# Performance work log

Hardware: AMD Instinct MI355X
Metric: run time of the kernel (lower is better)

## Reference

```python
import jax, jax.numpy as jnp
import numpy as np

V = 20000          # vocab size ('ALL')
E = 512            # embedding_dim
H = 1024           # rnn_hidden_size
LD = 256           # latent_dim
NL = 2             # num_rnn_layers_dec (hidden_factor = 2, unidirectional)
B = 32
S = 256
PAD = 0
CUT0 = 30          # cutoffs = [30, 100, 1000], div_value = 4.0
TAIL_SPECS = [(30, 100, 256), (100, 1000, 64), (1000, V, 16)]  # (low, high, proj_dim)


def setup_inputs() -> dict:
    key = jax.random.key(0)
    ks = jax.random.split(key, 24)
    w = lambda k, shp: (0.02 * jax.random.normal(k, shp)).astype(jnp.float32)

    z = jax.random.normal(ks[0], (B, LD), dtype=jnp.float32)
    emb = w(ks[1], (V, E))
    l2h_w = w(ks[2], (NL * H, LD))
    l2h_b = jnp.zeros((NL * H,), jnp.float32)
    # RNN layer 0 (input E) and layer 1 (input H)
    rnn0_wih = w(ks[3], (H, E)); rnn0_whh = w(ks[4], (H, H))
    rnn0_bih = jnp.zeros((H,), jnp.float32); rnn0_bhh = jnp.zeros((H,), jnp.float32)
    rnn1_wih = w(ks[5], (H, H)); rnn1_whh = w(ks[6], (H, H))
    rnn1_bih = jnp.zeros((H,), jnp.float32); rnn1_bhh = jnp.zeros((H,), jnp.float32)
    # adaptive softmax: head = 30 shortlist + 3 cluster logits
    head_w = w(ks[7], (CUT0 + 3, H))
    tail_p0 = w(ks[8], (256, H));  tail_w0 = w(ks[9], (70, 256))
    tail_p1 = w(ks[10], (64, H));  tail_w1 = w(ks[11], (900, 64))
    tail_p2 = w(ks[12], (16, H));  tail_w2 = w(ks[13], (V - 1000, 16))

    length = jax.random.randint(ks[14], (B,), 32, S + 1)
    pos = jnp.arange(S)[None, :]
    mask = pos < length[:, None]
    inp_seq = jax.random.randint(ks[15], (B, S), 4, V)
    inp_seq = jnp.where(mask, inp_seq, PAD)
    target_seq = jax.random.randint(ks[16], (B, S), 4, V)
    target_seq = jnp.where(mask, target_seq, PAD)

    return dict(z=z, emb=emb, l2h_w=l2h_w, l2h_b=l2h_b,
                rnn0_wih=rnn0_wih, rnn0_whh=rnn0_whh, rnn0_bih=rnn0_bih, rnn0_bhh=rnn0_bhh,
                rnn1_wih=rnn1_wih, rnn1_whh=rnn1_whh, rnn1_bih=rnn1_bih, rnn1_bhh=rnn1_bhh,
                head_w=head_w, tail_p0=tail_p0, tail_w0=tail_w0, tail_p1=tail_p1,
                tail_w1=tail_w1, tail_p2=tail_p2, tail_w2=tail_w2,
                inp_seq=inp_seq, target_seq=target_seq, length=length)


def _rnn_layer(x, h0, wih, whh, bih, bhh):
    # x: [B,S,D], h0: [B,H] -> [B,S,H]  (tanh vanilla RNN)
    def step(h, xt):
        h = jnp.tanh(xt @ wih.T + bih + h @ whh.T + bhh)
        return h, h
    _, ys = jax.lax.scan(step, h0, jnp.swapaxes(x, 0, 1))
    return jnp.swapaxes(ys, 0, 1)


def _adaptive_log_prob(x, head_w, tails):
    # x: [N,H] -> full log-probs [N,V] (AdaptiveLogSoftmaxWithLoss.log_prob)
    head_lp = jax.nn.log_softmax(x @ head_w.T, axis=-1)  # [N, 33]
    parts = [head_lp[:, :CUT0]]
    for i, (p, w) in enumerate(tails):
        clp = jax.nn.log_softmax((x @ p.T) @ w.T, axis=-1)
        parts.append(clp + head_lp[:, CUT0 + i][:, None])
    return jnp.concatenate(parts, axis=1)


def reference(z, emb, l2h_w, l2h_b,
              rnn0_wih, rnn0_whh, rnn0_bih, rnn0_bhh,
              rnn1_wih, rnn1_whh, rnn1_bih, rnn1_bhh,
              head_w, tail_p0, tail_w0, tail_p1, tail_w1, tail_p2, tail_w2,
              inp_seq, target_seq, length):
    # sort inputs by descending length (hidden is NOT sorted, as in the original)
    sorted_idx = jnp.argsort(-length)
    x = emb[inp_seq[sorted_idx]]                         # [B,S,E]
    hid = z @ l2h_w.T + l2h_b                            # [B, 2H]
    hidden = hid.reshape(NL, B, H)                       # torch .view(hidden_factor, B, H)
    h1 = _rnn_layer(x, hidden[0], rnn0_wih, rnn0_whh, rnn0_bih, rnn0_bhh)
    h2 = _rnn_layer(h1, hidden[1], rnn1_wih, rnn1_whh, rnn1_bih, rnn1_bhh)
    rev = jnp.argsort(sorted_idx)
    out = h2[rev].reshape(-1, H)                         # [N,H]
    tgt = target_seq.reshape(-1)                         # [N]
    lp = _adaptive_log_prob(out, head_w,
                            [(tail_p0, tail_w0), (tail_p1, tail_w1), (tail_p2, tail_w2)])
    nll = -jnp.take_along_axis(lp, tgt[:, None], axis=1)[:, 0]
    nll = jnp.where(tgt == PAD, 0.0, nll)
    return jnp.sum(nll)
```

## Files before the change

### kernel.cpp

```cpp
#include <hip/hip_runtime.h>
#include <hip/hip_bf16.h>
#include <math.h>

#define BB 32
#define SS 256
#define EE 512
#define HH 1024
#define LDM 256
#define NROW (BB*SS)
#define NWG 64

typedef __attribute__((ext_vector_type(8))) short bf16x8;
typedef __attribute__((ext_vector_type(4))) float f32x4;
typedef unsigned long long u64;

static __device__ inline unsigned short f2bf(float f){
  unsigned u = __float_as_uint(f);
  unsigned r = (u + 0x7fffu + ((u >> 16) & 1u)) >> 16;
  return (unsigned short)r;
}
static __device__ inline unsigned short f2bf_fast(float f){
  return (unsigned short)((__float_as_uint(f) + 0x8000u) >> 16);
}
static __device__ inline bf16x8 cvt8(float4 x, float4 y){
  union { ushort s[8]; bf16x8 v; } t;
  t.s[0]=f2bf_fast(x.x); t.s[1]=f2bf_fast(x.y); t.s[2]=f2bf_fast(x.z); t.s[3]=f2bf_fast(x.w);
  t.s[4]=f2bf_fast(y.x); t.s[5]=f2bf_fast(y.y); t.s[6]=f2bf_fast(y.z); t.s[7]=f2bf_fast(y.w);
  return t.v;
}
static __device__ inline unsigned packbf(float a, float b){
  return (unsigned)f2bf(a) | ((unsigned)f2bf(b) << 16);
}

static __device__ inline float ftanh(float x){
  float e = __expf(2.f*x);
  return 1.f - 2.f/(e + 1.f);
}

#define GLD(dst, p) asm volatile("global_load_dwordx4 %0, %1, off sc0 sc1" \
                                 : "=v"(dst) : "v"(p) : "memory")

static __device__ inline bf16x8 asbf(f32x4 x){
  union { f32x4 f; bf16x8 b; } u; u.f = x; return u.b;
}

__global__ void k_sort(const int* __restrict__ length, int* __restrict__ sorted_idx){
  int b = threadIdx.x;
  if (b >= BB) return;
  int lb = length[b];
  int r = 0;
  for (int o = 0; o < BB; ++o){
    int lo = length[o];
    if (lo > lb || (lo == lb && o < b)) ++r;
  }
  sorted_idx[r] = b;
}

__global__ void k_maps(const int* __restrict__ sorted_idx,
                       const int* __restrict__ inp_seq, const int* __restrict__ tgt_seq,
                       int* __restrict__ tokmap, int* __restrict__ tgtmap){
  int bs = blockIdx.x; int t = threadIdx.x;
  int b = sorted_idx[bs];
  tokmap[bs*SS + t] = inp_seq[b*SS + t];
  tgtmap[bs*SS + t] = tgt_seq[b*SS + t];
}

__global__ __launch_bounds__(256) void k_hid(const float* __restrict__ z,
        const float* __restrict__ w, const float* __restrict__ bias,
        ushort* __restrict__ hb0){
  int id = blockIdx.x*256 + threadIdx.x;
  int b = id >> 11, c = id & 2047;
  const float4* zr = (const float4*)(z + b*LDM);
  const float4* wr = (const float4*)(w + (size_t)c*LDM);
  float a0=0,a1=0,a2=0,a3=0;
  #pragma unroll 4
  for (int k=0;k<LDM/4;k++){ float4 zz=zr[k], ww=wr[k];
    a0+=zz.x*ww.x; a1+=zz.y*ww.y; a2+=zz.z*ww.z; a3+=zz.w*ww.w; }
  float val = a0+a1+a2+a3 + bias[c];
  int layer = id >> 15, bp = (id >> 10) & 31, j = id & 1023;
  hb0[(layer<<15) + ((j>>3)<<8) + (bp<<3) + (j&7)] = f2bf(val);
}

__global__ __launch_bounds__(256) void k_wcat(
    const float* __restrict__ head_w, const float* __restrict__ p0,
    const float* __restrict__ p1, const float* __restrict__ p2,
    float* __restrict__ wcat){
  int row = blockIdx.x; int t = threadIdx.x;
  float4* dst = (float4*)(wcat + (size_t)row*HH);
  const float* src;
  if      (row < 33)  src = head_w + (size_t)row*HH;
  else if (row < 289) src = p0 + (size_t)(row-33)*HH;
  else if (row < 353) src = p1 + (size_t)(row-289)*HH;
  else if (row < 369) src = p2 + (size_t)(row-353)*HH;
  else { dst[t] = make_float4(0.f,0.f,0.f,0.f); return; }
  dst[t] = ((const float4*)src)[t];
}

__global__ __launch_bounds__(256) void k_bin(
    const int* __restrict__ tgtmap, int* __restrict__ cnt,
    int* __restrict__ l0, int* __restrict__ l1, int* __restrict__ l2)
{
  int row = blockIdx.x*256 + threadIdx.x;
  int tgt = tgtmap[row];
  int ci = (tgt == 0) ? -1 : (tgt >= 1000) ? 2 : (tgt >= 100) ? 1 : (tgt >= 30) ? 0 : -1;
  int lane = threadIdx.x & 63;
  #pragma unroll
  for (int c = 0; c < 3; ++c){
    unsigned long long mask = __ballot(ci == c);
    int nc = __popcll(mask);
    int base = 0;
    if (lane == 0 && nc) base = atomicAdd(&cnt[c], nc);
    base = __shfl(base, 0);
    if (ci == c){
      int pos = __popcll(mask & ((1ull << lane) - 1ull));
      int* lst = (c == 0) ? l0 : (c == 1) ? l1 : l2;
      lst[base + pos] = row;
    }
  }
}

__global__ __launch_bounds__(256) void k_gemm_bf16(
    const float* __restrict__ A, int lda, const int* __restrict__ rowmap, int abf16,
    const float* __restrict__ Bm,
    const float* __restrict__ bias0, const float* __restrict__ bias1,
    float* __restrict__ C, int M, int N, int K)
{
  __shared__ ushort As[128*72];
  __shared__ ushort Bs[128*72];
  const int nt = blockIdx.x * 128, mt = blockIdx.y * 128;
  const int tid = threadIdx.x;
  const int wv = tid >> 6, ln = tid & 63;
  const int wm = wv & 1, wn = wv >> 1;
  const int lc = ln & 15, quad = ln >> 4;
  f32x4 acc[4][4] = {{{0.f,0.f,0.f,0.f}}};

  for (int s = 0; s < K; s += 64){
    __syncthreads();
    #pragma unroll
    for (int cc = 0; cc < 4; ++cc){
      int ch = tid*4 + cc;
      int r = ch >> 3, c = ch & 7;
      int ar = mt + r;
      if (abf16){
        const ushort* ap = (const ushort*)A + (size_t)ar*lda + s + c*8;
        *(bf16x8*)&As[r*72 + c*8] = *(const bf16x8*)ap;
      } else {
        const float* ap = A + (size_t)(rowmap ? rowmap[ar] : ar)*lda + s + c*8;
        float4 x = *(const float4*)ap, y = *(const float4*)(ap+4);
        *(bf16x8*)&As[r*72 + c*8] = cvt8(x, y);
      }
      int br = nt + r; if (br >= N) br = N - 1;
      const float* bp = Bm + (size_t)br*K + s + c*8;
      float4 bx = *(const float4*)bp, by = *(const float4*)(bp+4);
      *(bf16x8*)&Bs[r*72 + c*8] = cvt8(bx, by);
    }
    __syncthreads();
    #pragma unroll
    for (int kq = 0; kq < 2; ++kq){
      int cq = kq*4 + quad;
      bf16x8 af[4], bfv[4];
      #pragma unroll
      for (int i=0;i<4;i++) af[i]  = *(const bf16x8*)&As[(wm*64 + i*16 + lc)*72 + cq*8];
      #pragma unroll
      for (int j=0;j<4;j++) bfv[j] = *(const bf16x8*)&Bs[(wn*64 + j*16 + lc)*72 + cq*8];
      #pragma unroll
      for (int i=0;i<4;i++)
        #pragma unroll
        for (int j=0;j<4;j++)
          acc[i][j] = __builtin_amdgcn_mfma_f32_16x16x32_bf16(af[i], bfv[j], acc[i][j], 0, 0, 0);
    }
  }
  #pragma unroll
  for (int j=0;j<4;j++){
    int col = nt + wn*64 + j*16 + lc;
    if (col < N){
      float badd = (bias0 ? bias0[col] : 0.f) + (bias1 ? bias1[col] : 0.f);
      #pragma unroll
      for (int i=0;i<4;i++){
        int row = mt + wm*64 + i*16 + quad*4;
        #pragma unroll
        for (int r=0;r<4;r++)
          C[(size_t)(row+r)*N + col] = acc[i][j][r] + badd;
      }
    }
  }
}

__global__ __launch_bounds__(256, 1) void k_rnn_fused(
    const float* __restrict__ pre0, ushort* __restrict__ h2out,
    const float* __restrict__ w0hh, const float* __restrict__ w1ih,
    const float* __restrict__ w1hh,
    const float* __restrict__ b1ih, const float* __restrict__ b1hh,
    const ushort* __restrict__ hb0, ushort* __restrict__ hx, int* flags)
{
  __shared__ ushort w0F[16384], wiF[16384], whF[16384];
  __shared__ float red[4352];
  const int wg  = blockIdx.x;
  const int tid = threadIdx.x;
  const int j0  = wg * 16;
  int* ctr = flags + (wg & 7) * 32;

  for (int c = tid; c < 4096; c += 256){
    int rr = c >> 8, cc = (c & 255) * 4;
    int dst = ((cc >> 3)*16 + rr)*8 + (cc & 7);
    size_t srow = (size_t)(j0 + rr)*HH + cc;
    float4 w4; uint2 p;
    w4 = *(const float4*)&w0hh[srow];
    p.x = packbf(w4.x, w4.y); p.y = packbf(w4.z, w4.w);
    *(uint2*)&w0F[dst] = p;
    w4 = *(const float4*)&w1ih[srow];
    p.x = packbf(w4.x, w4.y); p.y = packbf(w4.z, w4.w);
    *(uint2*)&wiF[dst] = p;
    w4 = *(const float4*)&w1hh[srow];
    p.x = packbf(w4.x, w4.y); p.y = packbf(w4.z, w4.w);
    *(uint2*)&whF[dst] = p;
  }
  const int lane = tid & 63, wv = tid >> 6;
  const int col = lane & 15, quad = lane >> 4;
  const int ob = tid >> 3, oj = (tid << 1) & 15;

  float2 pre = *(const float2*)&pre0[((size_t)ob*SS + 0)*HH + j0 + oj];
  float2 pre2;
  pre2.x = b1ih[j0+oj]   + b1hh[j0+oj];
  pre2.y = b1ih[j0+oj+1] + b1hh[j0+oj+1];
  __syncthreads();

  for (int r = 0; r < SS; ++r){
    const u64* s1 = (const u64*)(r == 0 ? hb0 : hx + ((r-1)&1)*32768);
    const u64* s2 = (r == 0) ? (const u64*)hb0
                  : (const u64*)(r == 1 ? hb0 + 32768 : hx + (2 + (r&1))*32768);
    f32x4 a0r[8], a1r[8], c0r[8], c1r[8];
    #pragma unroll
    for (int ks = 0; ks < 8; ++ks){
      int kb = wv*32 + ks*4 + quad;
      const u64* p = s1 + (kb << 6) + (col << 1);
      GLD(a0r[ks], p);
      GLD(a1r[ks], p + 32);
    }
    if (r > 0){
      #pragma unroll
      for (int ks = 0; ks < 8; ++ks){
        int kb = wv*32 + ks*4 + quad;
        const u64* p = s2 + (kb << 6) + (col << 1);
        GLD(c0r[ks], p);
        GLD(c1r[ks], p + 32);
      }
    }
    asm volatile("s_waitcnt vmcnt(0)" ::: "memory");
    __builtin_amdgcn_sched_barrier(0);

    f32x4 accA0 = {0.f,0.f,0.f,0.f}, accA1 = {0.f,0.f,0.f,0.f};
    f32x4 accB0 = {0.f,0.f,0.f,0.f}, accB1 = {0.f,0.f,0.f,0.f};
    #pragma unroll
    for (int ks = 0; ks < 8; ++ks){
      int kb = wv*32 + ks*4 + quad;
      bf16x8 b0 = *(const bf16x8*)&w0F[(kb*16 + col)*8];
      accA0 = __builtin_amdgcn_mfma_f32_16x16x32_bf16(asbf(a0r[ks]), b0, accA0, 0, 0, 0);
      accA1 = __builtin_amdgcn_mfma_f32_16x16x32_bf16(asbf(a1r[ks]), b0, accA1, 0, 0, 0);
      bf16x8 bi = *(const bf16x8*)&wiF[(kb*16 + col)*8];
      accB0 = __builtin_amdgcn_mfma_f32_16x16x32_bf16(asbf(a0r[ks]), bi, accB0, 0, 0, 0);
      accB1 = __builtin_amdgcn_mfma_f32_16x16x32_bf16(asbf(a1r[ks]), bi, accB1, 0, 0, 0);
    }
    if (r > 0){
      #pragma unroll
      for (int ks = 0; ks < 8; ++ks){
        int kb = wv*32 + ks*4 + quad;
        bf16x8 bh = *(const bf16x8*)&whF[(kb*16 + col)*8];
        accB0 = __builtin_amdgcn_mfma_f32_16x16x32_bf16(asbf(c0r[ks]), bh, accB0, 0, 0, 0);
        accB1 = __builtin_amdgcn_mfma_f32_16x16x32_bf16(asbf(c1r[ks]), bh, accB1, 0, 0, 0);
      }
    }
    #pragma unroll
    for (int q = 0; q < 4; ++q){
      red[wv*544 + (quad*4 + q)*17 + col]             = accA0[q];
      red[wv*544 + (16 + quad*4 + q)*17 + col]        = accA1[q];
      red[2176 + wv*544 + (quad*4 + q)*17 + col]      = accB0[q];
      red[2176 + wv*544 + (16 + quad*4 + q)*17 + col] = accB1[q];
    }
    __syncthreads();

    int ro = ob*17 + oj;
    float s0 = red[ro]   + red[544 + ro]   + red[1088 + ro]   + red[1632 + ro];
    float s1v= red[ro+1] + red[544 + ro+1] + red[1088 + ro+1] + red[1632 + ro+1];
    float v0 = ftanh(pre.x + s0);
    float v1 = ftanh(pre.y + s1v);
    int k = j0 + oj;
    unsigned off = ((unsigned)(k >> 3) << 7) + ((unsigned)ob << 2) + ((unsigned)(k & 7) >> 1);
    __hip_atomic_store((unsigned*)(hx + (r&1)*32768) + off, packbf(v0, v1),
                       __ATOMIC_RELAXED, __HIP_MEMORY_SCOPE_AGENT);
    unsigned pk2 = 0;
    if (r > 0){
      float s2v = red[2176+ro]   + red[2720+ro]   + red[3264+ro]   + red[3808+ro];
      float s3v = red[2176+ro+1] + red[2720+ro+1] + red[3264+ro+1] + red[3808+ro+1];
      pk2 = packbf(ftanh(pre2.x + s2v), ftanh(pre2.y + s3v));
      __hip_atomic_store((unsigned*)(hx + (2 + ((r-1)&1))*32768) + off, pk2,
                         __ATOMIC_RELAXED, __HIP_MEMORY_SCOPE_AGENT);
    }
    asm volatile("s_waitcnt vmcnt(0)" ::: "memory");
    __syncthreads();
    if (tid == 0)
      __hip_atomic_fetch_add(ctr, 1, __ATOMIC_RELAXED, __HIP_MEMORY_SCOPE_AGENT);

    if (r > 0)
      *((unsigned*)h2out + (((size_t)ob*SS + (r-1))*HH + j0 + oj) / 2) = pk2;
    int tn = (r + 1 < SS) ? r + 1 : SS - 1;
    pre = *(const float2*)&pre0[((size_t)ob*SS + tn)*HH + j0 + oj];

    if (tid < 8){
      int tv = 8 * (r + 1);
      while (__hip_atomic_load(flags + tid*32, __ATOMIC_RELAXED,
                               __HIP_MEMORY_SCOPE_AGENT) < tv) {}
    }
    __syncthreads();
  }

  {
    const u64* s1 = (const u64*)(hx + 32768);
    const u64* s2 = (const u64*)(hx + 2*32768);
    f32x4 a0r[8], a1r[8], c0r[8], c1r[8];
    #pragma unroll
    for (int ks = 0; ks < 8; ++ks){
      int kb = wv*32 + ks*4 + quad;
      const u64* p1 = s1 + (kb << 6) + (col << 1);
      GLD(a0r[ks], p1); GLD(a1r[ks], p1 + 32);
      const u64* p2 = s2 + (kb << 6) + (col << 1);
      GLD(c0r[ks], p2); GLD(c1r[ks], p2 + 32);
    }
    asm volatile("s_waitcnt vmcnt(0)" ::: "memory");
    __builtin_amdgcn_sched_barrier(0);
    f32x4 accB0 = {0.f,0.f,0.f,0.f}, accB1 = {0.f,0.f,0.f,0.f};
    #pragma unroll
    for (int ks = 0; ks < 8; ++ks){
      int kb = wv*32 + ks*4 + quad;
      bf16x8 bi = *(const bf16x8*)&wiF[(kb*16 + col)*8];
      accB0 = __builtin_amdgcn_mfma_f32_16x16x32_bf16(asbf(a0r[ks]), bi, accB0, 0, 0, 0);
      accB1 = __builtin_amdgcn_mfma_f32_16x16x32_bf16(asbf(a1r[ks]), bi, accB1, 0, 0, 0);
      bf16x8 bh = *(const bf16x8*)&whF[(kb*16 + col)*8];
      accB0 = __builtin_amdgcn_mfma_f32_16x16x32_bf16(asbf(c0r[ks]), bh, accB0, 0, 0, 0);
      accB1 = __builtin_amdgcn_mfma_f32_16x16x32_bf16(asbf(c1r[ks]), bh, accB1, 0, 0, 0);
    }
    #pragma unroll
    for (int q = 0; q < 4; ++q){
      red[wv*544 + (quad*4 + q)*17 + col]      = accB0[q];
      red[wv*544 + (16 + quad*4 + q)*17 + col] = accB1[q];
    }
    __syncthreads();
    int ro = ob*17 + oj;
    float s2v = red[ro]   + red[544 + ro]   + red[1088 + ro]   + red[1632 + ro];
    float s3v = red[ro+1] + red[544 + ro+1] + red[1088 + ro+1] + red[1632 + ro+1];
    *((unsigned*)h2out + (((size_t)ob*SS + (SS-1))*HH + j0 + oj) / 2) =
        packbf(ftanh(pre2.x + s2v), ftanh(pre2.y + s3v));
  }
}

__global__ __launch_bounds__(256) void k_cluster(
    const float* __restrict__ combo, int off, int ld, int Kp,
    const float* __restrict__ W, int Nc,
    const int* __restrict__ rowlist, const int* __restrict__ cntp, int ci,
    float* __restrict__ stats)
{
  __shared__ float ps[4][4][256];
  int lane = threadIdx.x & 63;
  int wvl  = threadIdx.x >> 6;
  int n0 = (blockIdx.x*4 + wvl) * 4;
  int count = cntp[ci];
  int rows[4];
  #pragma unroll
  for (int r=0;r<4;r++){
    rows[r] = (n0 + r < count) ? rowlist[n0 + r] : -1;
    if (rows[r] >= 0)
      for (int k=lane;k<Kp;k+=64)
        ps[wvl][r][k] = combo[(size_t)rows[r]*ld + off + k];
  }
  __syncthreads();
  if (rows[0] < 0) return;

  float mx[4], sm[4];
  #pragma unroll
  for (int r=0;r<4;r++){ mx[r]=-1e30f; sm[r]=0.f; }
  for (int n=lane; n<Nc; n+=64){
    const float* wr = W + (size_t)n*Kp;
    float l[4]={0.f,0.f,0.f,0.f};
    for (int k=0;k<Kp;k+=4){
      float4 w4 = *(const float4*)(wr+k);
      #pragma unroll
      for (int r=0;r<4;r++){
        l[r] += w4.x*ps[wvl][r][k] + w4.y*ps[wvl][r][k+1]
              + w4.z*ps[wvl][r][k+2] + w4.w*ps[wvl][r][k+3];
      }
    }
    #pragma unroll
    for (int r=0;r<4;r++){
      float nm = fmaxf(mx[r], l[r]);
      sm[r] = sm[r]*__expf(mx[r]-nm) + __expf(l[r]-nm);
      mx[r] = nm;
    }
  }
  #pragma unroll
  for (int r=0;r<4;r++){
    for (int off2=32; off2; off2>>=1){
      float om = __shfl_down(mx[r], off2);
      float os = __shfl_down(sm[r], off2);
      float nm = fmaxf(mx[r], om);
      sm[r] = sm[r]*__expf(mx[r]-nm) + os*__expf(om-nm);
      mx[r] = nm;
    }
    if (lane==0 && rows[r] >= 0){
      stats[(size_t)rows[r]*6 + ci*2 + 0] = mx[r];
      stats[(size_t)rows[r]*6 + ci*2 + 1] = sm[r];
    }
  }
}

__global__ __launch_bounds__(256) void k_tlogit(
    const int* __restrict__ tgtmap, const float* __restrict__ combo,
    const float* __restrict__ w0, const float* __restrict__ w1, const float* __restrict__ w2,
    float* __restrict__ tlogit)
{
  int lane = threadIdx.x & 63;
  int row = (blockIdx.x * 256 + threadIdx.x) >> 6;
  int tgt = tgtmap[row];
  float acc = 0.f;
  const float* pr = nullptr; const float* wr = nullptr; int Kp = 0;
  const float* crow = combo + (size_t)row*384;
  if      (tgt >= 1000){ pr = crow + 353; wr = w2 + (size_t)(tgt-1000)*16;  Kp=16;  }
  else if (tgt >= 100) { pr = crow + 289; wr = w1 + (size_t)(tgt-100)*64;   Kp=64;  }
  else if (tgt >= 30)  { pr = crow + 33;  wr = w0 + (size_t)(tgt-30)*256;   Kp=256; }
  for (int k=lane; k<Kp; k+=64) acc += pr[k]*wr[k];
  for (int off=32; off; off>>=1) acc += __shfl_down(acc, off);
  if (lane==0) tlogit[row] = acc;
}

__global__ __launch_bounds__(256) void k_final(
    const float* __restrict__ combo, const float* __restrict__ stats,
    const float* __restrict__ tlogit, const int* __restrict__ tgtmap,
    float* __restrict__ out)
{
  int row = blockIdx.x*256 + threadIdx.x;
  int tgt = tgtmap[row];
  float nll = 0.f;
  if (tgt != 0){
    const float* hrow = combo + (size_t)row*384;
    float m = hrow[0];
    #pragma unroll
    for (int i=1;i<33;i++) m = fmaxf(m, hrow[i]);
    float s = 0.f;
    #pragma unroll
    for (int i=0;i<33;i++) s += __expf(hrow[i]-m);
    float lse = __logf(s) + m;
    int ci = (tgt>=1000) ? 2 : (tgt>=100) ? 1 : (tgt>=30) ? 0 : -1;
    if (ci < 0){
      nll = lse - hrow[tgt];
    } else {
      float cm = stats[(size_t)row*6 + ci*2 + 0];
      float cs = stats[(size_t)row*6 + ci*2 + 1];
      nll = lse - hrow[30+ci] + (__logf(cs) + cm - tlogit[row]);
    }
  }
  float v = nll;
  for (int off=32; off; off>>=1) v += __shfl_down(v, off);
  __shared__ float wsum[4];
  int lane = threadIdx.x & 63, wv = threadIdx.x >> 6;
  if (lane==0) wsum[wv] = v;
  __syncthreads();
  if (threadIdx.x==0) atomicAdd(out, wsum[0]+wsum[1]+wsum[2]+wsum[3]);
}

extern "C" void kernel_launch(void* const* d_in, const int* in_sizes, int n_in,
                              void* d_out, int out_size, void* d_ws, size_t ws_size,
                              hipStream_t stream)
{
  const float* z      = (const float*)d_in[0];
  const float* emb    = (const float*)d_in[1];
  const float* l2h_w  = (const float*)d_in[2];
  const float* l2h_b  = (const float*)d_in[3];
  const float* w0ih   = (const float*)d_in[4];
  const float* w0hh   = (const float*)d_in[5];
  const float* b0ih   = (const float*)d_in[6];
  const float* b0hh   = (const float*)d_in[7];
  const float* w1ih   = (const float*)d_in[8];
  const float* w1hh   = (const float*)d_in[9];
  const float* b1ih   = (const float*)d_in[10];
  const float* b1hh   = (const float*)d_in[11];
  const float* head_w = (const float*)d_in[12];
  const float* p0     = (const float*)d_in[13];
  const float* tw0    = (const float*)d_in[14];
  const float* p1     = (const float*)d_in[15];
  const float* tw1    = (const float*)d_in[16];
  const float* p2     = (const float*)d_in[17];
  const float* tw2    = (const float*)d_in[18];
  const int* inp_seq  = (const int*)d_in[19];
  const int* tgt_seq  = (const int*)d_in[20];
  const int* length   = (const int*)d_in[21];

  float* ws   = (float*)d_ws;
  ushort* hb0 = (ushort*)ws;
  ushort* hx  = hb0 + 65536;
  float* bufA = ws + 98304;
  ushort* hbB = (ushort*)(bufA + (size_t)NROW*HH);
  int*   ibuf = (int*)(hbB + (size_t)NROW*HH);
  int* sorted_idx = ibuf;
  int* tokmap = ibuf + 32;
  int* tgtmap = tokmap + NROW;
  int* flags  = tgtmap + NROW;
  int* bincnt = flags + 512;
  int* blist0 = bincnt + 32;
  int* blist1 = blist0 + NROW;
  int* blist2 = blist1 + NROW;
  float* combo = bufA;
  float* stats = bufA + (size_t)NROW*384;
  float* tlog  = stats + (size_t)NROW*6;
  float* wcat  = tlog + NROW;

  float* outF = (float*)d_out;
  hipMemsetAsync(outF, 0, sizeof(float), stream);
  hipMemsetAsync(flags, 0, 544*sizeof(int), stream);

  k_sort<<<1, 32, 0, stream>>>(length, sorted_idx);
  k_maps<<<32, 256, 0, stream>>>(sorted_idx, inp_seq, tgt_seq, tokmap, tgtmap);
  k_hid<<<256, 256, 0, stream>>>(z, l2h_w, l2h_b, hb0);
  k_bin<<<32, 256, 0, stream>>>(tgtmap, bincnt, blist0, blist1, blist2);

  k_gemm_bf16<<<dim3(HH/128, NROW/128), 256, 0, stream>>>(emb, EE, tokmap, 0, w0ih,
                                                          b0ih, b0hh, bufA, NROW, HH, EE);
  k_rnn_fused<<<NWG, 256, 0, stream>>>(bufA, hbB, w0hh, w1ih, w1hh, b1ih, b1hh,
                                       hb0, hx, flags);

  k_wcat<<<384, 256, 0, stream>>>(head_w, p0, p1, p2, wcat);
  k_gemm_bf16<<<dim3(3, NROW/128), 256, 0, stream>>>((const float*)hbB, HH, nullptr, 1,
                                                     wcat, nullptr, nullptr,
                                                     combo, NROW, 384, HH);

  k_cluster<<<NROW/16, 256, 0, stream>>>(combo, 33,  384, 256, tw0, 70,
                                         blist0, bincnt, 0, stats);
  k_cluster<<<NROW/16, 256, 0, stream>>>(combo, 289, 384, 64,  tw1, 900,
                                         blist1, bincnt, 1, stats);
  k_cluster<<<NROW/16, 256, 0, stream>>>(combo, 353, 384, 16,  tw2, 19000,
                                         blist2, bincnt, 2, stats);
  k_tlogit<<<NROW/4, 256, 0, stream>>>(tgtmap, combo, tw0, tw1, tw2, tlog);
  k_final<<<NROW/256, 256, 0, stream>>>(combo, stats, tlog, tgtmap, outF);
}
```

Measured before the change: 1.529 ms.

## Split fused two-layer RNN into separate layer-1 and layer-2 workgroup roles

The persistent RNN kernel used 64 workgroups that each computed both layers in a skewed wavefront. It now launches 128 workgroups, 64 for layer 1 and 64 for layer 2, which run as a pipeline linked by per-role flag counters and a triple-buffered h1 ring. This halves the per-step MFMA and load work on each workgroup and shortens each step's critical path. In exchange it needs twice as many CUs to be co-resident, adds cross-role spin waits, and enlarges the workspace to hold the extra buffers.

```diff
diff --git a/kernel.cpp b/kernel.cpp
--- a/kernel.cpp
+++ b/kernel.cpp
@@ -8,7 +8,6 @@
 #define HH 1024
 #define LDM 256
 #define NROW (BB*SS)
-#define NWG 64
 
 typedef __attribute__((ext_vector_type(8))) short bf16x8;
 typedef __attribute__((ext_vector_type(4))) float f32x4;
@@ -186,7 +185,7 @@
   }
 }
 
-__global__ __launch_bounds__(256, 1) void k_rnn_fused(
+__global__ __launch_bounds__(256, 1) void k_rnn_split(
     const float* __restrict__ pre0, ushort* __restrict__ h2out,
     const float* __restrict__ w0hh, const float* __restrict__ w1ih,
     const float* __restrict__ w1hh,
@@ -194,162 +193,160 @@
     const ushort* __restrict__ hb0, ushort* __restrict__ hx, int* flags)
 {
   __shared__ ushort w0F[16384], wiF[16384], whF[16384];
-  __shared__ float red[4352];
+  __shared__ float red[2176];
   const int wg  = blockIdx.x;
   const int tid = threadIdx.x;
-  const int j0  = wg * 16;
-  int* ctr = flags + (wg & 7) * 32;
+  const bool roleL2 = wg >= 64;
+  const int cw  = roleL2 ? wg - 64 : wg;
+  const int j0  = cw * 16;
+  int* myctr = flags + (roleL2 ? 256 : 0) + (cw & 7) * 32;
 
   for (int c = tid; c < 4096; c += 256){
     int rr = c >> 8, cc = (c & 255) * 4;
     int dst = ((cc >> 3)*16 + rr)*8 + (cc & 7);
     size_t srow = (size_t)(j0 + rr)*HH + cc;
     float4 w4; uint2 p;
-    w4 = *(const float4*)&w0hh[srow];
-    p.x = packbf(w4.x, w4.y); p.y = packbf(w4.z, w4.w);
-    *(uint2*)&w0F[dst] = p;
-    w4 = *(const float4*)&w1ih[srow];
-    p.x = packbf(w4.x, w4.y); p.y = packbf(w4.z, w4.w);
-    *(uint2*)&wiF[dst] = p;
-    w4 = *(const float4*)&w1hh[srow];
-    p.x = packbf(w4.x, w4.y); p.y = packbf(w4.z, w4.w);
-    *(uint2*)&whF[dst] = p;
+    if (!roleL2){
+      w4 = *(const float4*)&w0hh[srow];
+      p.x = packbf(w4.x, w4.y); p.y = packbf(w4.z, w4.w);
+      *(uint2*)&w0F[dst] = p;
+    } else {
+      w4 = *(const float4*)&w1ih[srow];
+      p.x = packbf(w4.x, w4.y); p.y = packbf(w4.z, w4.w);
+      *(uint2*)&wiF[dst] = p;
+      w4 = *(const float4*)&w1hh[srow];
+      p.x = packbf(w4.x, w4.y); p.y = packbf(w4.z, w4.w);
+      *(uint2*)&whF[dst] = p;
+    }
   }
   const int lane = tid & 63, wv = tid >> 6;
   const int col = lane & 15, quad = lane >> 4;
   const int ob = tid >> 3, oj = (tid << 1) & 15;
-
-  float2 pre = *(const float2*)&pre0[((size_t)ob*SS + 0)*HH + j0 + oj];
-  float2 pre2;
-  pre2.x = b1ih[j0+oj]   + b1hh[j0+oj];
-  pre2.y = b1ih[j0+oj+1] + b1hh[j0+oj+1];
-  __syncthreads();
-
-  for (int r = 0; r < SS; ++r){
-    const u64* s1 = (const u64*)(r == 0 ? hb0 : hx + ((r-1)&1)*32768);
-    const u64* s2 = (r == 0) ? (const u64*)hb0
-                  : (const u64*)(r == 1 ? hb0 + 32768 : hx + (2 + (r&1))*32768);
-    f32x4 a0r[8], a1r[8], c0r[8], c1r[8];
-    #pragma unroll
-    for (int ks = 0; ks < 8; ++ks){
-      int kb = wv*32 + ks*4 + quad;
-      const u64* p = s1 + (kb << 6) + (col << 1);
-      GLD(a0r[ks], p);
-      GLD(a1r[ks], p + 32);
-    }
-    if (r > 0){
+  const int ro = ob*17 + oj;
+  const int k = j0 + oj;
+  const unsigned off = ((unsigned)(k >> 3) << 7) + ((unsigned)ob << 2) + ((unsigned)(k & 7) >> 1);
+  ushort* h1buf = hx;
+  ushort* h2buf = hx + 3*32768;
+
+  if (!roleL2){
+    float2 pre = *(const float2*)&pre0[((size_t)ob*SS + 0)*HH + j0 + oj];
+    __syncthreads();
+    for (int t = 0; t < SS; ++t){
+      const u64* s1 = (const u64*)(t == 0 ? hb0 : h1buf + ((t+2)%3)*32768);
+      f32x4 a0r[8], a1r[8];
       #pragma unroll
       for (int ks = 0; ks < 8; ++ks){
         int kb = wv*32 + ks*4 + quad;
-        const u64* p = s2 + (kb << 6) + (col << 1);
+        const u64* p = s1 + (kb << 6) + (col << 1);
+        GLD(a0r[ks], p);
+        GLD(a1r[ks], p + 32);
+      }
+      asm volatile("s_waitcnt vmcnt(0)" ::: "memory");
+      __builtin_amdgcn_sched_barrier(0);
+
+      f32x4 acc0 = {0.f,0.f,0.f,0.f}, acc1 = {0.f,0.f,0.f,0.f};
+      #pragma unroll
+      for (int ks = 0; ks < 8; ++ks){
+        int kb = wv*32 + ks*4 + quad;
+        bf16x8 b0 = *(const bf16x8*)&w0F[(kb*16 + col)*8];
+        acc0 = __builtin_amdgcn_mfma_f32_16x16x32_bf16(asbf(a0r[ks]), b0, acc0, 0, 0, 0);
+        acc1 = __builtin_amdgcn_mfma_f32_16x16x32_bf16(asbf(a1r[ks]), b0, acc1, 0, 0, 0);
+      }
+      #pragma unroll
+      for (int q = 0; q < 4; ++q){
+        red[wv*544 + (quad*4 + q)*17 + col]      = acc0[q];
+        red[wv*544 + (16 + quad*4 + q)*17 + col] = acc1[q];
+      }
+      __syncthreads();
+      float s0 = red[ro]   + red[544 + ro]   + red[1088 + ro]   + red[1632 + ro];
+      float s1v= red[ro+1] + red[544 + ro+1] + red[1088 + ro+1] + red[1632 + ro+1];
+      unsigned pk = packbf(ftanh(pre.x + s0), ftanh(pre.y + s1v));
+      __hip_atomic_store((unsigned*)(h1buf + (t%3)*32768) + off, pk,
+                         __ATOMIC_RELAXED, __HIP_MEMORY_SCOPE_AGENT);
+      asm volatile("s_waitcnt vmcnt(0)" ::: "memory");
+      __syncthreads();
+      if (tid == 0)
+        __hip_atomic_fetch_add(myctr, 1, __ATOMIC_RELAXED, __HIP_MEMORY_SCOPE_AGENT);
+
+      int tn = (t + 1 < SS) ? t + 1 : SS - 1;
+      pre = *(const float2*)&pre0[((size_t)ob*SS + tn)*HH + j0 + oj];
+
+      if (t < SS - 1 && tid < 16){
+        int tv = (tid < 8) ? 8*(t+1) : 8*(t-1);
+        const int* fp = flags + ((tid < 8) ? 0 : 256) + (tid & 7)*32;
+        if (tv > 0)
+          while (__hip_atomic_load(fp, __ATOMIC_RELAXED, __HIP_MEMORY_SCOPE_AGENT) < tv) {}
+      }
+      __syncthreads();
+    }
+  } else {
+    float2 pre2;
+    pre2.x = b1ih[j0+oj]   + b1hh[j0+oj];
+    pre2.y = b1ih[j0+oj+1] + b1hh[j0+oj+1];
+    __syncthreads();
+    if (tid < 8){
+      while (__hip_atomic_load(flags + tid*32, __ATOMIC_RELAXED,
+                               __HIP_MEMORY_SCOPE_AGENT) < 8) {}
+    }
+    __syncthreads();
+    for (int s = 0; s < SS; ++s){
+      const u64* sa = (const u64*)(h1buf + (s%3)*32768);
+      const u64* sc = (const u64*)(s == 0 ? hb0 + 32768
+                                          : h2buf + ((s+1)&1)*32768);
+      f32x4 a0r[8], a1r[8], c0r[8], c1r[8];
+      #pragma unroll
+      for (int ks = 0; ks < 8; ++ks){
+        int kb = wv*32 + ks*4 + quad;
+        const u64* p = sa + (kb << 6) + (col << 1);
+        GLD(a0r[ks], p);
+        GLD(a1r[ks], p + 32);
+      }
+      #pragma unroll
+      for (int ks = 0; ks < 8; ++ks){
+        int kb = wv*32 + ks*4 + quad;
+        const u64* p = sc + (kb << 6) + (col << 1);
         GLD(c0r[ks], p);
         GLD(c1r[ks], p + 32);
       }
-    }
-    asm volatile("s_waitcnt vmcnt(0)" ::: "memory");
-    __builtin_amdgcn_sched_barrier(0);
-
-    f32x4 accA0 = {0.f,0.f,0.f,0.f}, accA1 = {0.f,0.f,0.f,0.f};
-    f32x4 accB0 = {0.f,0.f,0.f,0.f}, accB1 = {0.f,0.f,0.f,0.f};
-    #pragma unroll
-    for (int ks = 0; ks < 8; ++ks){
-      int kb = wv*32 + ks*4 + quad;
-      bf16x8 b0 = *(const bf16x8*)&w0F[(kb*16 + col)*8];
-      accA0 = __builtin_amdgcn_mfma_f32_16x16x32_bf16(asbf(a0r[ks]), b0, accA0, 0, 0, 0);
-      accA1 = __builtin_amdgcn_mfma_f32_16x16x32_bf16(asbf(a1r[ks]), b0, accA1, 0, 0, 0);
-      bf16x8 bi = *(const bf16x8*)&wiF[(kb*16 + col)*8];
-      accB0 = __builtin_amdgcn_mfma_f32_16x16x32_bf16(asbf(a0r[ks]), bi, accB0, 0, 0, 0);
-      accB1 = __builtin_amdgcn_mfma_f32_16x16x32_bf16(asbf(a1r[ks]), bi, accB1, 0, 0, 0);
-    }
-    if (r > 0){
+      asm volatile("s_waitcnt vmcnt(0)" ::: "memory");
+      __builtin_amdgcn_sched_barrier(0);
+
+      f32x4 acc0 = {0.f,0.f,0.f,0.f}, acc1 = {0.f,0.f,0.f,0.f};
       #pragma unroll
       for (int ks = 0; ks < 8; ++ks){
         int kb = wv*32 + ks*4 + quad;
+        bf16x8 bi = *(const bf16x8*)&wiF[(kb*16 + col)*8];
+        acc0 = __builtin_amdgcn_mfma_f32_16x16x32_bf16(asbf(a0r[ks]), bi, acc0, 0, 0, 0);
+        acc1 = __builtin_amdgcn_mfma_f32_16x16x32_bf16(asbf(a1r[ks]), bi, acc1, 0, 0, 0);
         bf16x8 bh = *(const bf16x8*)&whF[(kb*16 + col)*8];
-        accB0 = __builtin_amdgcn_mfma_f32_16x16x32_bf16(asbf(c0r[ks]), bh, accB0, 0, 0, 0);
-        accB1 = __builtin_amdgcn_mfma_f32_16x16x32_bf16(asbf(c1r[ks]), bh, accB1, 0, 0, 0);
-      }
-    }
-    #pragma unroll
-    for (int q = 0; q < 4; ++q){
-      red[wv*544 + (quad*4 + q)*17 + col]             = accA0[q];
-      red[wv*544 + (16 + quad*4 + q)*17 + col]        = accA1[q];
-      red[2176 + wv*544 + (quad*4 + q)*17 + col]      = accB0[q];
-      red[2176 + wv*544 + (16 + quad*4 + q)*17 + col] = accB1[q];
-    }
-    __syncthreads();
-
-    int ro = ob*17 + oj;
-    float s0 = red[ro]   + red[544 + ro]   + red[1088 + ro]   + red[1632 + ro];
-    float s1v= red[ro+1] + red[544 + ro+1] + red[1088 + ro+1] + red[1632 + ro+1];
-    float v0 = ftanh(pre.x + s0);
-    float v1 = ftanh(pre.y + s1v);
-    int k = j0 + oj;
-    unsigned off = ((unsigned)(k >> 3) << 7) + ((unsigned)ob << 2) + ((unsigned)(k & 7) >> 1);
-    __hip_atomic_store((unsigned*)(hx + (r&1)*32768) + off, packbf(v0, v1),
-                       __ATOMIC_RELAXED, __HIP_MEMORY_SCOPE_AGENT);
-    unsigned pk2 = 0;
-    if (r > 0){
-      float s2v = red[2176+ro]   + red[2720+ro]   + red[3264+ro]   + red[3808+ro];
-      float s3v = red[2176+ro+1] + red[2720+ro+1] + red[3264+ro+1] + red[3808+ro+1];
-      pk2 = packbf(ftanh(pre2.x + s2v), ftanh(pre2.y + s3v));
-      __hip_atomic_store((unsigned*)(hx + (2 + ((r-1)&1))*32768) + off, pk2,
+        acc0 = __builtin_amdgcn_mfma_f32_16x16x32_bf16(asbf(c0r[ks]), bh, acc0, 0, 0, 0);
+        acc1 = __builtin_amdgcn_mfma_f32_16x16x32_bf16(asbf(c1r[ks]), bh, acc1, 0, 0, 0);
+      }
+      #pragma unroll
+      for (int q = 0; q < 4; ++q){
+        red[wv*544 + (quad*4 + q)*17 + col]      = acc0[q];
+        red[wv*544 + (16 + quad*4 + q)*17 + col] = acc1[q];
+      }
+      __syncthreads();
+      float s2v = red[ro]   + red[544 + ro]   + red[1088 + ro]   + red[1632 + ro];
+      float s3v = red[ro+1] + red[544 + ro+1] + red[1088 + ro+1] + red[1632 + ro+1];
+      unsigned pk2 = packbf(ftanh(pre2.x + s2v), ftanh(pre2.y + s3v));
+      __hip_atomic_store((unsigned*)(h2buf + (s&1)*32768) + off, pk2,
                          __ATOMIC_RELAXED, __HIP_MEMORY_SCOPE_AGENT);
-    }
-    asm volatile("s_waitcnt vmcnt(0)" ::: "memory");
-    __syncthreads();
-    if (tid == 0)
-      __hip_atomic_fetch_add(ctr, 1, __ATOMIC_RELAXED, __HIP_MEMORY_SCOPE_AGENT);
-
-    if (r > 0)
-      *((unsigned*)h2out + (((size_t)ob*SS + (r-1))*HH + j0 + oj) / 2) = pk2;
-    int tn = (r + 1 < SS) ? r + 1 : SS - 1;
-    pre = *(const float2*)&pre0[((size_t)ob*SS + tn)*HH + j0 + oj];
-
-    if (tid < 8){
-      int tv = 8 * (r + 1);
-      while (__hip_atomic_load(flags + tid*32, __ATOMIC_RELAXED,
-                               __HIP_MEMORY_SCOPE_AGENT) < tv) {}
-    }
-    __syncthreads();
-  }
-
-  {
-    const u64* s1 = (const u64*)(hx + 32768);
-    const u64* s2 = (const u64*)(hx + 2*32768);
-    f32x4 a0r[8], a1r[8], c0r[8], c1r[8];
-    #pragma unroll
-    for (int ks = 0; ks < 8; ++ks){
-      int kb = wv*32 + ks*4 + quad;
-      const u64* p1 = s1 + (kb << 6) + (col << 1);
-      GLD(a0r[ks], p1); GLD(a1r[ks], p1 + 32);
-      const u64* p2 = s2 + (kb << 6) + (col << 1);
-      GLD(c0r[ks], p2); GLD(c1r[ks], p2 + 32);
-    }
-    asm volatile("s_waitcnt vmcnt(0)" ::: "memory");
-    __builtin_amdgcn_sched_barrier(0);
-    f32x4 accB0 = {0.f,0.f,0.f,0.f}, accB1 = {0.f,0.f,0.f,0.f};
-    #pragma unroll
-    for (int ks = 0; ks < 8; ++ks){
-      int kb = wv*32 + ks*4 + quad;
-      bf16x8 bi = *(const bf16x8*)&wiF[(kb*16 + col)*8];
-      accB0 = __builtin_amdgcn_mfma_f32_16x16x32_bf16(asbf(a0r[ks]), bi, accB0, 0, 0, 0);
-      accB1 = __builtin_amdgcn_mfma_f32_16x16x32_bf16(asbf(a1r[ks]), bi, accB1, 0, 0, 0);
-      bf16x8 bh = *(const bf16x8*)&whF[(kb*16 + col)*8];
-      accB0 = __builtin_amdgcn_mfma_f32_16x16x32_bf16(asbf(c0r[ks]), bh, accB0, 0, 0, 0);
-      accB1 = __builtin_amdgcn_mfma_f32_16x16x32_bf16(asbf(c1r[ks]), bh, accB1, 0, 0, 0);
-    }
-    #pragma unroll
-    for (int q = 0; q < 4; ++q){
-      red[wv*544 + (quad*4 + q)*17 + col]      = accB0[q];
-      red[wv*544 + (16 + quad*4 + q)*17 + col] = accB1[q];
-    }
-    __syncthreads();
-    int ro = ob*17 + oj;
-    float s2v = red[ro]   + red[544 + ro]   + red[1088 + ro]   + red[1632 + ro];
-    float s3v = red[ro+1] + red[544 + ro+1] + red[1088 + ro+1] + red[1632 + ro+1];
-    *((unsigned*)h2out + (((size_t)ob*SS + (SS-1))*HH + j0 + oj) / 2) =
-        packbf(ftanh(pre2.x + s2v), ftanh(pre2.y + s3v));
+      asm volatile("s_waitcnt vmcnt(0)" ::: "memory");
+      __syncthreads();
+      if (tid == 0)
+        __hip_atomic_fetch_add(myctr, 1, __ATOMIC_RELAXED, __HIP_MEMORY_SCOPE_AGENT);
+
+      *((unsigned*)h2out + (((size_t)ob*SS + s)*HH + j0 + oj) / 2) = pk2;
+
+      if (s < SS - 1 && tid < 16){
+        int tv = (tid < 8) ? 8*(s+2) : 8*(s+1);
+        const int* fp = flags + ((tid < 8) ? 0 : 256) + (tid & 7)*32;
+        while (__hip_atomic_load(fp, __ATOMIC_RELAXED, __HIP_MEMORY_SCOPE_AGENT) < tv) {}
+      }
+      __syncthreads();
+    }
   }
 }
 
@@ -496,7 +493,7 @@
   float* ws   = (float*)d_ws;
   ushort* hb0 = (ushort*)ws;
   ushort* hx  = hb0 + 65536;
-  float* bufA = ws + 98304;
+  float* bufA = ws + 114688;
   ushort* hbB = (ushort*)(bufA + (size_t)NROW*HH);
   int*   ibuf = (int*)(hbB + (size_t)NROW*HH);
   int* sorted_idx = ibuf;
@@ -523,7 +520,7 @@
 
   k_gemm_bf16<<<dim3(HH/128, NROW/128), 256, 0, stream>>>(emb, EE, tokmap, 0, w0ih,
                                                           b0ih, b0hh, bufA, NROW, HH, EE);
-  k_rnn_fused<<<NWG, 256, 0, stream>>>(bufA, hbB, w0hh, w1ih, w1hh, b1ih, b1hh,
+  k_rnn_split<<<128, 256, 0, stream>>>(bufA, hbB, w0hh, w1ih, w1hh, b1ih, b1hh,
                                        hb0, hx, flags);
 
   k_wcat<<<384, 256, 0, stream>>>(head_w, p0, p1, p2, wcat);
```

New measurement: 1.516 ms. Within noise of the previous version (-0.8%).
